# Performance work log

Hardware: AMD Instinct MI355X
Metric: run time of the kernel (lower is better)

The kernel has to match this reference:

```python
import jax, jax.numpy as jnp
import numpy as np

B, S, D, R = 256, 512, 128, 2048
H = 0.5  # integration step


def setup_inputs() -> dict:
    key = jax.random.key(0)
    ks = jax.random.split(key, 14)
    u = lambda k, shape, lo, hi: jax.random.uniform(k, shape, jnp.float32, lo, hi)
    bd, br = 1.0 / np.sqrt(D), 1.0 / np.sqrt(R)
    return {
        "inputs": jax.random.normal(ks[0], (B, S, D), jnp.float32),
        # input oscillator params (size D)
        "omega_in": u(ks[1], (D,), 1.0, 3.0),
        "gamma_in": u(ks[2], (D,), 0.1, 0.5),
        "alpha_in": u(ks[3], (D,), 0.5, 1.5),
        # input projection Linear(D -> R), torch layout [out, in]
        "W_proj": u(ks[4], (R, D), -bd, bd),
        "b_proj": u(ks[5], (R,), -bd, bd),
        # fixed reservoir oscillator params (size R)
        "omega_res": u(ks[6], (R,), 1.0, 3.0),
        "gamma_res": u(ks[7], (R,), 0.1, 0.5),
        "alpha_res": u(ks[8], (R,), 0.5, 1.5),
        # output oscillator params (size R)
        "omega_out": u(ks[9], (R,), 1.0, 3.0),
        "gamma_out": u(ks[10], (R,), 0.1, 0.5),
        "alpha_out": u(ks[11], (R,), 0.5, 1.5),
        # readout Linear(R -> D)
        "W_read": u(ks[12], (D, R), -br, br),
        "b_read": u(ks[13], (D,), -br, br),
    }


def _osc_step(f, x, y, omega, gamma, alpha):
    # x' = x + h*y ; y' = y + h*(alpha*f - 2|gamma|*y - |omega|^2 * x), clamped to [-5,5]
    accel = alpha * f - 2.0 * jnp.abs(gamma) * y - jnp.abs(omega) ** 2 * x
    x_new = jnp.clip(x + H * y, -5.0, 5.0)
    y_new = jnp.clip(y + H * accel, -5.0, 5.0)
    return x_new, y_new


def reference(inputs, omega_in, gamma_in, alpha_in, W_proj, b_proj,
              omega_res, gamma_res, alpha_res, omega_out, gamma_out, alpha_out,
              W_read, b_read):
    inputs_t = jnp.transpose(inputs, (1, 0, 2))  # [S, B, D]

    def step(carry, inp_t):
        x_in, y_in, x_res, y_res, x_out, y_out = carry
        x_in, y_in = _osc_step(inp_t, x_in, y_in, omega_in, gamma_in, alpha_in)
        proj = x_in @ W_proj.T + b_proj                      # [B, R]
        x_res, y_res = _osc_step(proj, x_res, y_res, omega_res, gamma_res, alpha_res)
        x_out, y_out = _osc_step(x_res, x_out, y_out, omega_out, gamma_out, alpha_out)
        pred = x_out @ W_read.T + b_read                     # [B, D]
        mse_out = jnp.mean((x_out - x_res) ** 2)             # scalar per step
        return (x_in, y_in, x_res, y_res, x_out, y_out), (pred, x_in, mse_out)

    z_d = jnp.zeros((B, D), inputs.dtype)
    z_r = jnp.zeros((B, R), inputs.dtype)
    carry0 = (z_d, z_d, z_r, z_r, z_r, z_r)
    _, (preds_t, x_in_seq, mse_out_seq) = jax.lax.scan(step, carry0, inputs_t)

    preds = jnp.transpose(preds_t, (1, 0, 2))  # [B, S, D]
    # pc_loss_in = sum_{t<S-1} mean((x_in(t) - inputs(t+1))^2)
    pc_loss_in = jnp.sum(jnp.mean((x_in_seq[:-1] - inputs_t[1:]) ** 2, axis=(1, 2)))
    pc_loss_out = jnp.sum(mse_out_seq)
    return preds, pc_loss_in, pc_loss_out
```

## Files before the change

### kernel.cpp

```cpp
#include <hip/hip_runtime.h>
#include <hip/hip_bf16.h>

#define Bn 256
#define Sn 512
#define Dn 128
#define Rn 2048
#define TB 32
#define NBLK (Sn / TB)
#define LDX 136
#define LDPs 1028
#define LDI 132
#define RG 1024

using bf16_t = __hip_bfloat16;
typedef short bf16x8 __attribute__((ext_vector_type(8)));
typedef float f32x4 __attribute__((ext_vector_type(4)));
typedef float f32x2 __attribute__((ext_vector_type(2)));

__device__ __forceinline__ f32x2 clip2(f32x2 v) {
  v = __builtin_elementwise_max(v, (f32x2)(-5.f));
  v = __builtin_elementwise_min(v, (f32x2)(5.f));
  return v;
}

__device__ __forceinline__ unsigned bf16rne(float f) {
  const unsigned u = __float_as_uint(f);
  return (u + 0x7fffu + ((u >> 16) & 1u)) >> 16;
}
__device__ __forceinline__ unsigned pack_bf16(f32x2 v) {
  return (bf16rne(v.y) << 16) | (bf16rne(v.x) & 0xffffu);
}

__global__ __launch_bounds__(256) void k_prep(const float* __restrict__ Wp,
                                              const float* __restrict__ Wr,
                                              bf16_t* __restrict__ Wp_b,
                                              bf16_t* __restrict__ Wr_b,
                                              float* __restrict__ losses) {
  const int i = blockIdx.x * 256 + threadIdx.x;
  Wp_b[i] = __float2bfloat16(Wp[i]);
  Wr_b[i] = __float2bfloat16(Wr[i]);
  if (i == 0) { losses[0] = 0.f; losses[1] = 0.f; }
}

__global__ __launch_bounds__(256) void k_zero(float* __restrict__ preds,
                                              const float* __restrict__ br) {
  const int i = blockIdx.x * 256 + threadIdx.x;
  const f32x4 bv = *(const f32x4*)(br + (i & 31) * 4);
  *((f32x4*)preds + i) = bv;
}

__global__ __launch_bounds__(512, 4) void k_fused(
    const float* __restrict__ inp,
    const float* __restrict__ om_i, const float* __restrict__ ga_i,
    const float* __restrict__ al_i,
    const bf16_t* __restrict__ Wp, const float* __restrict__ bp,
    const float* __restrict__ omr, const float* __restrict__ gar,
    const float* __restrict__ alr,
    const float* __restrict__ omo, const float* __restrict__ gao,
    const float* __restrict__ alo,
    const bf16_t* __restrict__ Wr,
    float* __restrict__ preds, float* __restrict__ losses) {
  __shared__ bf16_t Xs[TB * LDX];
  __shared__ bf16_t PX[TB * LDPs];
  __shared__ float bpS[RG];
  __shared__ float smi[8], smo[8];

  const int tid = threadIdx.x;
  const int b = blockIdx.x >> 1, g = blockIdx.x & 1;
  const int rbase = g * RG;
  const int wv = tid >> 6, lane = tid & 63;
  const int lr = lane & 15, lq = lane >> 4;

  for (int i = tid; i < RG; i += 512) bpS[i] = bp[rbase + i];

  float xi = 0.f, yi = 0.f, pc_in = 0.f;
  float w2i = 0.f, g2i = 0.f, ai = 0.f;
  if (tid < Dn) {
    w2i = om_i[tid] * om_i[tid];
    g2i = 2.f * fabsf(ga_i[tid]);
    ai = al_i[tid];
  }
  const float* inpb = inp + (size_t)b * Sn * Dn;

  const int rl = tid * 2;
  f32x2 xr = (f32x2)0.f, yr = (f32x2)0.f, xo = (f32x2)0.f, yo = (f32x2)0.f;
  f32x2 w2r, g2r, arv, w2o, g2o, aov;
  {
    f32x2 t;
    t = *(const f32x2*)(omr + rbase + rl); w2r = t * t;
    t = *(const f32x2*)(gar + rbase + rl); g2r = __builtin_elementwise_abs(t) * 2.f;
    arv = *(const f32x2*)(alr + rbase + rl);
    t = *(const f32x2*)(omo + rbase + rl); w2o = t * t;
    t = *(const f32x2*)(gao + rbase + rl); g2o = __builtin_elementwise_abs(t) * 2.f;
    aov = *(const f32x2*)(alo + rbase + rl);
  }
  f32x2 pc_out2 = (f32x2)0.f;

  float* Is = (float*)PX;

  __syncthreads();

  for (int blk = 0; blk < NBLK; ++blk) {
    const int t0 = blk * TB;

    {
      const float* src = inpb + (size_t)t0 * Dn;
      for (int i = tid; i < (TB * Dn) / 4; i += 512) {
        const int row = i >> 5, c4 = (i & 31) * 4;
        f32x4 v = __builtin_nontemporal_load((const f32x4*)(src + (size_t)row * Dn + c4));
        *(f32x4*)&Is[row * LDI + c4] = v;
      }
    }
    __syncthreads();

    if (tid < Dn) {
#pragma unroll
      for (int tt = 0; tt < TB; ++tt) {
        const float f = Is[tt * LDI + tid];
        if (t0 + tt > 0) { const float e = xi - f; pc_in += e * e; }
        const float accel = ai * f - g2i * yi - w2i * xi;
        const float xn = fminf(fmaxf(xi + 0.5f * yi, -5.f), 5.f);
        const float yn = fminf(fmaxf(yi + 0.5f * accel, -5.f), 5.f);
        Xs[tt * LDX + tid] = __float2bfloat16(xn);
        xi = xn; yi = yn;
      }
    }
    __syncthreads();

    {
      bf16x8 af[2][4];
#pragma unroll
      for (int i = 0; i < 2; ++i)
#pragma unroll
        for (int k = 0; k < 4; ++k)
          af[i][k] = *(const bf16x8*)&Xs[(i * 16 + lr) * LDX + k * 32 + lq * 8];

      const int lb = wv * 128;
      const bf16_t* wp_base = Wp + (size_t)(rbase + lb + lr) * Dn + lq * 8;
      bf16x8 bf[2][4];
#pragma unroll
      for (int k = 0; k < 4; ++k) {
        bf[0][k] = *(const bf16x8*)(wp_base + (size_t)0 * 16 * Dn + k * 32);
        bf[1][k] = *(const bf16x8*)(wp_base + (size_t)1 * 16 * Dn + k * 32);
      }
      for (int j = 0; j < 8; ++j) {
        const int pb = j & 1;
        f32x4 acc[2] = {(f32x4)0.f, (f32x4)0.f};
#pragma unroll
        for (int k = 0; k < 4; ++k) {
          acc[0] = __builtin_amdgcn_mfma_f32_16x16x32_bf16(af[0][k], bf[pb][k], acc[0], 0, 0, 0);
          acc[1] = __builtin_amdgcn_mfma_f32_16x16x32_bf16(af[1][k], bf[pb][k], acc[1], 0, 0, 0);
        }
        if (j + 2 < 8) {
#pragma unroll
          for (int k = 0; k < 4; ++k)
            bf[pb][k] = *(const bf16x8*)(wp_base + (size_t)(j + 2) * 16 * Dn + k * 32);
        }
        const int cl = lb + j * 16 + lr;
        const float bv = bpS[cl];
#pragma unroll
        for (int i = 0; i < 2; ++i)
#pragma unroll
          for (int r = 0; r < 4; ++r)
            PX[(i * 16 + lq * 4 + r) * LDPs + cl] = __float2bfloat16(acc[i][r] + bv);
      }
    }
    __syncthreads();

    {
      unsigned pk = *(unsigned*)&PX[0 * LDPs + rl];
      for (int tt = 0; tt < TB; ++tt) {
        unsigned pk_n = pk;
        if (tt + 1 < TB) pk_n = *(unsigned*)&PX[(tt + 1) * LDPs + rl];
        f32x2 pv;
        pv.x = __uint_as_float(pk << 16);
        pv.y = __uint_as_float(pk & 0xffff0000u);
        f32x2 acr = arv * pv - g2r * yr - w2r * xr;
        f32x2 xrn = clip2(xr + yr * 0.5f);
        f32x2 yrn = clip2(yr + acr * 0.5f);
        f32x2 aco = aov * xrn - g2o * yo - w2o * xo;
        f32x2 xon = clip2(xo + yo * 0.5f);
        f32x2 yon = clip2(yo + aco * 0.5f);
        f32x2 e = xon - xrn;
        pc_out2 += e * e;
        xr = xrn; yr = yrn; xo = xon; yo = yon;
        *(unsigned*)&PX[tt * LDPs + rl] = pack_bf16(xon);
        pk = pk_n;
      }
    }
    __syncthreads();

    {
      const int d0 = wv * 16;
      const bf16_t* wr_base = Wr + (size_t)(d0 + lr) * Rn + rbase + lq * 8;
      f32x4 acc[2][2] = {{(f32x4)0.f, (f32x4)0.f}, {(f32x4)0.f, (f32x4)0.f}};
      bf16x8 bcur = *(const bf16x8*)(wr_base);
#pragma unroll 2
      for (int k0 = 0; k0 < RG; k0 += 32) {
        bf16x8 bnxt = bcur;
        if (k0 + 32 < RG) bnxt = *(const bf16x8*)(wr_base + k0 + 32);
        const int par = (k0 >> 5) & 1;
        bf16x8 a0 = *(const bf16x8*)&PX[(0 + lr) * LDPs + k0 + lq * 8];
        bf16x8 a1 = *(const bf16x8*)&PX[(16 + lr) * LDPs + k0 + lq * 8];
        acc[0][par] = __builtin_amdgcn_mfma_f32_16x16x32_bf16(a0, bcur, acc[0][par], 0, 0, 0);
        acc[1][par] = __builtin_amdgcn_mfma_f32_16x16x32_bf16(a1, bcur, acc[1][par], 0, 0, 0);
        bcur = bnxt;
      }
      float* outb = preds + (size_t)b * Sn * Dn + (size_t)t0 * Dn;
      const int col = d0 + lr;
#pragma unroll
      for (int i = 0; i < 2; ++i) {
        f32x4 a = acc[i][0] + acc[i][1];
#pragma unroll
        for (int r = 0; r < 4; ++r) {
          const int row = i * 16 + lq * 4 + r;
          atomicAdd(outb + (size_t)row * Dn + col, a[r]);
        }
      }
    }
    __syncthreads();
  }

  float vi = pc_in;
  float vo = pc_out2.x + pc_out2.y;
#pragma unroll
  for (int o = 32; o > 0; o >>= 1) {
    vi += __shfl_down(vi, o, 64);
    vo += __shfl_down(vo, o, 64);
  }
  if (lane == 0) { smi[wv] = vi; smo[wv] = vo; }
  __syncthreads();
  if (tid == 0) {
    float si = 0.f, so = 0.f;
#pragma unroll
    for (int w = 0; w < 8; ++w) { si += smi[w]; so += smo[w]; }
    if (g == 0) atomicAdd(losses + 0, si * (1.f / ((float)Bn * (float)Dn)));
    atomicAdd(losses + 1, so * (1.f / ((float)Bn * (float)Rn)));
  }
}

extern "C" void kernel_launch(void* const* d_in, const int* in_sizes, int n_in,
                              void* d_out, int out_size, void* d_ws, size_t ws_size,
                              hipStream_t stream) {
  const float* inputs    = (const float*)d_in[0];
  const float* omega_in  = (const float*)d_in[1];
  const float* gamma_in  = (const float*)d_in[2];
  const float* alpha_in  = (const float*)d_in[3];
  const float* W_proj    = (const float*)d_in[4];
  const float* b_proj    = (const float*)d_in[5];
  const float* omega_res = (const float*)d_in[6];
  const float* gamma_res = (const float*)d_in[7];
  const float* alpha_res = (const float*)d_in[8];
  const float* omega_out = (const float*)d_in[9];
  const float* gamma_out = (const float*)d_in[10];
  const float* alpha_out = (const float*)d_in[11];
  const float* W_read    = (const float*)d_in[12];
  const float* b_read    = (const float*)d_in[13];

  float* out = (float*)d_out;
  float* losses = out + (size_t)Bn * Sn * Dn;

  bf16_t* Wp_b = (bf16_t*)d_ws;
  bf16_t* Wr_b = Wp_b + (size_t)Rn * Dn;

  k_prep<<<1024, 256, 0, stream>>>(W_proj, W_read, Wp_b, Wr_b, losses);
  k_zero<<<(Bn * Sn * Dn / 4) / 256, 256, 0, stream>>>(out, b_read);
  k_fused<<<Bn * 2, 512, 0, stream>>>(inputs, omega_in, gamma_in, alpha_in,
                                      Wp_b, b_proj,
                                      omega_res, gamma_res, alpha_res,
                                      omega_out, gamma_out, alpha_out,
                                      Wr_b, out, losses);
}
```

Baseline: 675.8 us.

## Use one 1024-thread block per batch row, dropping atomics and zero-init kernel

Each batch element is now processed by a single 1024-thread block covering the full reservoir width, instead of two 512-thread blocks that each handled half of it. Because one block now owns each readout output, the partial-sum atomicAdds and the separate bias-fill kernel are replaced by direct nontemporal stores with the bias added in place. The next input tile is also prefetched into registers during the readout phase. The trade-offs are half as many blocks, a larger shared-memory footprint (PX doubles in size), and 1024-thread blocks that may lower occupancy.

After: 952.3 us. 1.41x slower.

```diff
diff --git a/kernel.cpp b/kernel.cpp
--- a/kernel.cpp
+++ b/kernel.cpp
@@ -8,9 +8,10 @@
 #define TB 32
 #define NBLK (Sn / TB)
 #define LDX 136
-#define LDPs 1028
+#define LDP 2052
 #define LDI 132
-#define RG 1024
+#define NT 1024
+#define NW 16
 
 using bf16_t = __hip_bfloat16;
 typedef short bf16x8 __attribute__((ext_vector_type(8)));
@@ -42,14 +43,7 @@
   if (i == 0) { losses[0] = 0.f; losses[1] = 0.f; }
 }
 
-__global__ __launch_bounds__(256) void k_zero(float* __restrict__ preds,
-                                              const float* __restrict__ br) {
-  const int i = blockIdx.x * 256 + threadIdx.x;
-  const f32x4 bv = *(const f32x4*)(br + (i & 31) * 4);
-  *((f32x4*)preds + i) = bv;
-}
-
-__global__ __launch_bounds__(512, 4) void k_fused(
+__global__ __launch_bounds__(1024, 4) void k_fused(
     const float* __restrict__ inp,
     const float* __restrict__ om_i, const float* __restrict__ ga_i,
     const float* __restrict__ al_i,
@@ -58,20 +52,19 @@
     const float* __restrict__ alr,
     const float* __restrict__ omo, const float* __restrict__ gao,
     const float* __restrict__ alo,
-    const bf16_t* __restrict__ Wr,
+    const bf16_t* __restrict__ Wr, const float* __restrict__ br,
     float* __restrict__ preds, float* __restrict__ losses) {
   __shared__ bf16_t Xs[TB * LDX];
-  __shared__ bf16_t PX[TB * LDPs];
-  __shared__ float bpS[RG];
-  __shared__ float smi[8], smo[8];
+  __shared__ bf16_t PX[TB * LDP];
+  __shared__ float bpS[Rn];
+  __shared__ float smi[NW], smo[NW];
 
   const int tid = threadIdx.x;
-  const int b = blockIdx.x >> 1, g = blockIdx.x & 1;
-  const int rbase = g * RG;
+  const int b = blockIdx.x;
   const int wv = tid >> 6, lane = tid & 63;
   const int lr = lane & 15, lq = lane >> 4;
 
-  for (int i = tid; i < RG; i += 512) bpS[i] = bp[rbase + i];
+  for (int i = tid; i < Rn; i += NT) bpS[i] = bp[i];
 
   float xi = 0.f, yi = 0.f, pc_in = 0.f;
   float w2i = 0.f, g2i = 0.f, ai = 0.f;
@@ -87,30 +80,31 @@
   f32x2 w2r, g2r, arv, w2o, g2o, aov;
   {
     f32x2 t;
-    t = *(const f32x2*)(omr + rbase + rl); w2r = t * t;
-    t = *(const f32x2*)(gar + rbase + rl); g2r = __builtin_elementwise_abs(t) * 2.f;
-    arv = *(const f32x2*)(alr + rbase + rl);
-    t = *(const f32x2*)(omo + rbase + rl); w2o = t * t;
-    t = *(const f32x2*)(gao + rbase + rl); g2o = __builtin_elementwise_abs(t) * 2.f;
-    aov = *(const f32x2*)(alo + rbase + rl);
+    t = *(const f32x2*)(omr + rl); w2r = t * t;
+    t = *(const f32x2*)(gar + rl); g2r = __builtin_elementwise_abs(t) * 2.f;
+    arv = *(const f32x2*)(alr + rl);
+    t = *(const f32x2*)(omo + rl); w2o = t * t;
+    t = *(const f32x2*)(gao + rl); g2o = __builtin_elementwise_abs(t) * 2.f;
+    aov = *(const f32x2*)(alo + rl);
   }
   f32x2 pc_out2 = (f32x2)0.f;
 
+  const int dj = wv & 7, di = wv >> 3, d0 = dj * 16;
+  const float bco = br[d0 + lr];
+  const bf16_t* wr_base = Wr + (size_t)(d0 + lr) * Rn + lq * 8;
+
   float* Is = (float*)PX;
+  const int srow = tid >> 5, sc4 = (tid & 31) * 4;
+
+  f32x4 stg = __builtin_nontemporal_load(
+      (const f32x4*)(inpb + (size_t)srow * Dn + sc4));
 
   __syncthreads();
 
   for (int blk = 0; blk < NBLK; ++blk) {
     const int t0 = blk * TB;
 
-    {
-      const float* src = inpb + (size_t)t0 * Dn;
-      for (int i = tid; i < (TB * Dn) / 4; i += 512) {
-        const int row = i >> 5, c4 = (i & 31) * 4;
-        f32x4 v = __builtin_nontemporal_load((const f32x4*)(src + (size_t)row * Dn + c4));
-        *(f32x4*)&Is[row * LDI + c4] = v;
-      }
-    }
+    *(f32x4*)&Is[srow * LDI + sc4] = stg;
     __syncthreads();
 
     if (tid < Dn) {
@@ -136,7 +130,7 @@
           af[i][k] = *(const bf16x8*)&Xs[(i * 16 + lr) * LDX + k * 32 + lq * 8];
 
       const int lb = wv * 128;
-      const bf16_t* wp_base = Wp + (size_t)(rbase + lb + lr) * Dn + lq * 8;
+      const bf16_t* wp_base = Wp + (size_t)(lb + lr) * Dn + lq * 8;
       bf16x8 bf[2][4];
 #pragma unroll
       for (int k = 0; k < 4; ++k) {
@@ -162,16 +156,16 @@
         for (int i = 0; i < 2; ++i)
 #pragma unroll
           for (int r = 0; r < 4; ++r)
-            PX[(i * 16 + lq * 4 + r) * LDPs + cl] = __float2bfloat16(acc[i][r] + bv);
+            PX[(i * 16 + lq * 4 + r) * LDP + cl] = __float2bfloat16(acc[i][r] + bv);
       }
     }
     __syncthreads();
 
     {
-      unsigned pk = *(unsigned*)&PX[0 * LDPs + rl];
+      unsigned pk = *(unsigned*)&PX[0 * LDP + rl];
       for (int tt = 0; tt < TB; ++tt) {
         unsigned pk_n = pk;
-        if (tt + 1 < TB) pk_n = *(unsigned*)&PX[(tt + 1) * LDPs + rl];
+        if (tt + 1 < TB) pk_n = *(unsigned*)&PX[(tt + 1) * LDP + rl];
         f32x2 pv;
         pv.x = __uint_as_float(pk << 16);
         pv.y = __uint_as_float(pk & 0xffff0000u);
@@ -184,38 +178,34 @@
         f32x2 e = xon - xrn;
         pc_out2 += e * e;
         xr = xrn; yr = yrn; xo = xon; yo = yon;
-        *(unsigned*)&PX[tt * LDPs + rl] = pack_bf16(xon);
+        *(unsigned*)&PX[tt * LDP + rl] = pack_bf16(xon);
         pk = pk_n;
       }
     }
     __syncthreads();
 
     {
-      const int d0 = wv * 16;
-      const bf16_t* wr_base = Wr + (size_t)(d0 + lr) * Rn + rbase + lq * 8;
-      f32x4 acc[2][2] = {{(f32x4)0.f, (f32x4)0.f}, {(f32x4)0.f, (f32x4)0.f}};
+      if (blk + 1 < NBLK)
+        stg = __builtin_nontemporal_load(
+            (const f32x4*)(inpb + (size_t)(t0 + TB) * Dn + (size_t)srow * Dn + sc4));
+
+      f32x4 acc[2] = {(f32x4)0.f, (f32x4)0.f};
       bf16x8 bcur = *(const bf16x8*)(wr_base);
 #pragma unroll 2
-      for (int k0 = 0; k0 < RG; k0 += 32) {
+      for (int k0 = 0; k0 < Rn; k0 += 32) {
         bf16x8 bnxt = bcur;
-        if (k0 + 32 < RG) bnxt = *(const bf16x8*)(wr_base + k0 + 32);
+        if (k0 + 32 < Rn) bnxt = *(const bf16x8*)(wr_base + k0 + 32);
+        bf16x8 a = *(const bf16x8*)&PX[(di * 16 + lr) * LDP + k0 + lq * 8];
         const int par = (k0 >> 5) & 1;
-        bf16x8 a0 = *(const bf16x8*)&PX[(0 + lr) * LDPs + k0 + lq * 8];
-        bf16x8 a1 = *(const bf16x8*)&PX[(16 + lr) * LDPs + k0 + lq * 8];
-        acc[0][par] = __builtin_amdgcn_mfma_f32_16x16x32_bf16(a0, bcur, acc[0][par], 0, 0, 0);
-        acc[1][par] = __builtin_amdgcn_mfma_f32_16x16x32_bf16(a1, bcur, acc[1][par], 0, 0, 0);
+        acc[par] = __builtin_amdgcn_mfma_f32_16x16x32_bf16(a, bcur, acc[par], 0, 0, 0);
         bcur = bnxt;
       }
       float* outb = preds + (size_t)b * Sn * Dn + (size_t)t0 * Dn;
-      const int col = d0 + lr;
-#pragma unroll
-      for (int i = 0; i < 2; ++i) {
-        f32x4 a = acc[i][0] + acc[i][1];
-#pragma unroll
-        for (int r = 0; r < 4; ++r) {
-          const int row = i * 16 + lq * 4 + r;
-          atomicAdd(outb + (size_t)row * Dn + col, a[r]);
-        }
+      const f32x4 s = acc[0] + acc[1];
+#pragma unroll
+      for (int r = 0; r < 4; ++r) {
+        const int row = di * 16 + lq * 4 + r;
+        __builtin_nontemporal_store(s[r] + bco, outb + (size_t)row * Dn + d0 + lr);
       }
     }
     __syncthreads();
@@ -233,8 +223,8 @@
   if (tid == 0) {
     float si = 0.f, so = 0.f;
 #pragma unroll
-    for (int w = 0; w < 8; ++w) { si += smi[w]; so += smo[w]; }
-    if (g == 0) atomicAdd(losses + 0, si * (1.f / ((float)Bn * (float)Dn)));
+    for (int w = 0; w < NW; ++w) { si += smi[w]; so += smo[w]; }
+    atomicAdd(losses + 0, si * (1.f / ((float)Bn * (float)Dn)));
     atomicAdd(losses + 1, so * (1.f / ((float)Bn * (float)Rn)));
   }
 }
@@ -264,10 +254,9 @@
   bf16_t* Wr_b = Wp_b + (size_t)Rn * Dn;
 
   k_prep<<<1024, 256, 0, stream>>>(W_proj, W_read, Wp_b, Wr_b, losses);
-  k_zero<<<(Bn * Sn * Dn / 4) / 256, 256, 0, stream>>>(out, b_read);
-  k_fused<<<Bn * 2, 512, 0, stream>>>(inputs, omega_in, gamma_in, alpha_in,
-                                      Wp_b, b_proj,
-                                      omega_res, gamma_res, alpha_res,
-                                      omega_out, gamma_out, alpha_out,
-                                      Wr_b, out, losses);
-}
+  k_fused<<<Bn, NT, 0, stream>>>(inputs, omega_in, gamma_in, alpha_in,
+                                 Wp_b, b_proj,
+                                 omega_res, gamma_res, alpha_res,
+                                 omega_out, gamma_out, alpha_out,
+                                 Wr_b, b_read, out, losses);
+}
```

## Defer readout GEMM into next block to overlap with input oscillator, drop barriers

Applied to the files above, without the earlier changes.

The readout GEMM for the previous 32-step block now runs in the next iteration, while threads 0-127 integrate the input oscillator; a final call handles the last block. Since each wave's projection columns match the columns its own threads use in the reservoir recurrence, the barrier between those two phases is removed. The input staging through shared memory and its barrier are also removed, with threads reading the inputs straight from global memory. The projection bias is added in fp32 registers during the recurrence instead of being read from shared memory before bf16 rounding, and the block-index mapping now spreads the two R-halves across the grid. Together these cut barriers per block and keep the otherwise idle waves busy, at the cost of more register pressure and uncached global loads inside the serial input loop.

New measurement: 699.6 us. +3.5%, slower.

```diff
diff --git a/kernel.cpp b/kernel.cpp
--- a/kernel.cpp
+++ b/kernel.cpp
@@ -9,7 +9,6 @@
 #define NBLK (Sn / TB)
 #define LDX 136
 #define LDPs 1028
-#define LDI 132
 #define RG 1024
 
 using bf16_t = __hip_bfloat16;
@@ -62,16 +61,13 @@
     float* __restrict__ preds, float* __restrict__ losses) {
   __shared__ bf16_t Xs[TB * LDX];
   __shared__ bf16_t PX[TB * LDPs];
-  __shared__ float bpS[RG];
   __shared__ float smi[8], smo[8];
 
   const int tid = threadIdx.x;
-  const int b = blockIdx.x >> 1, g = blockIdx.x & 1;
+  const int b = blockIdx.x & 255, g = blockIdx.x >> 8;
   const int rbase = g * RG;
   const int wv = tid >> 6, lane = tid & 63;
   const int lr = lane & 15, lq = lane >> 4;
-
-  for (int i = tid; i < RG; i += 512) bpS[i] = bp[rbase + i];
 
   float xi = 0.f, yi = 0.f, pc_in = 0.f;
   float w2i = 0.f, g2i = 0.f, ai = 0.f;
@@ -84,7 +80,7 @@
 
   const int rl = tid * 2;
   f32x2 xr = (f32x2)0.f, yr = (f32x2)0.f, xo = (f32x2)0.f, yo = (f32x2)0.f;
-  f32x2 w2r, g2r, arv, w2o, g2o, aov;
+  f32x2 w2r, g2r, arv, w2o, g2o, aov, bpv;
   {
     f32x2 t;
     t = *(const f32x2*)(omr + rbase + rl); w2r = t * t;
@@ -93,30 +89,47 @@
     t = *(const f32x2*)(omo + rbase + rl); w2o = t * t;
     t = *(const f32x2*)(gao + rbase + rl); g2o = __builtin_elementwise_abs(t) * 2.f;
     aov = *(const f32x2*)(alo + rbase + rl);
+    bpv = *(const f32x2*)(bp + rbase + rl);
   }
   f32x2 pc_out2 = (f32x2)0.f;
 
-  float* Is = (float*)PX;
-
-  __syncthreads();
+  const bf16_t* wp_base = Wp + (size_t)(rbase + wv * 128 + lr) * Dn + lq * 8;
+  const int d0 = wv * 16;
+  const bf16_t* wr_base = Wr + (size_t)(d0 + lr) * Rn + rbase + lq * 8;
+
+  auto phaseD = [&](int tp0) {
+    f32x4 acc[2][2] = {{(f32x4)0.f, (f32x4)0.f}, {(f32x4)0.f, (f32x4)0.f}};
+    bf16x8 bcur = *(const bf16x8*)(wr_base);
+#pragma unroll 2
+    for (int k0 = 0; k0 < RG; k0 += 32) {
+      bf16x8 bnxt = bcur;
+      if (k0 + 32 < RG) bnxt = *(const bf16x8*)(wr_base + k0 + 32);
+      const int par = (k0 >> 5) & 1;
+      bf16x8 a0 = *(const bf16x8*)&PX[(0 + lr) * LDPs + k0 + lq * 8];
+      bf16x8 a1 = *(const bf16x8*)&PX[(16 + lr) * LDPs + k0 + lq * 8];
+      acc[0][par] = __builtin_amdgcn_mfma_f32_16x16x32_bf16(a0, bcur, acc[0][par], 0, 0, 0);
+      acc[1][par] = __builtin_amdgcn_mfma_f32_16x16x32_bf16(a1, bcur, acc[1][par], 0, 0, 0);
+      bcur = bnxt;
+    }
+    float* outb = preds + (size_t)b * Sn * Dn + (size_t)tp0 * Dn;
+#pragma unroll
+    for (int i = 0; i < 2; ++i) {
+      f32x4 s = acc[i][0] + acc[i][1];
+#pragma unroll
+      for (int r = 0; r < 4; ++r) {
+        const int row = i * 16 + lq * 4 + r;
+        atomicAdd(outb + (size_t)row * Dn + d0 + lr, s[r]);
+      }
+    }
+  };
 
   for (int blk = 0; blk < NBLK; ++blk) {
     const int t0 = blk * TB;
 
-    {
-      const float* src = inpb + (size_t)t0 * Dn;
-      for (int i = tid; i < (TB * Dn) / 4; i += 512) {
-        const int row = i >> 5, c4 = (i & 31) * 4;
-        f32x4 v = __builtin_nontemporal_load((const f32x4*)(src + (size_t)row * Dn + c4));
-        *(f32x4*)&Is[row * LDI + c4] = v;
-      }
-    }
-    __syncthreads();
-
     if (tid < Dn) {
 #pragma unroll
       for (int tt = 0; tt < TB; ++tt) {
-        const float f = Is[tt * LDI + tid];
+        const float f = inpb[(size_t)(t0 + tt) * Dn + tid];
         if (t0 + tt > 0) { const float e = xi - f; pc_in += e * e; }
         const float accel = ai * f - g2i * yi - w2i * xi;
         const float xn = fminf(fmaxf(xi + 0.5f * yi, -5.f), 5.f);
@@ -125,6 +138,7 @@
         xi = xn; yi = yn;
       }
     }
+    if (blk > 0) phaseD(t0 - TB);
     __syncthreads();
 
     {
@@ -135,37 +149,33 @@
         for (int k = 0; k < 4; ++k)
           af[i][k] = *(const bf16x8*)&Xs[(i * 16 + lr) * LDX + k * 32 + lq * 8];
 
-      const int lb = wv * 128;
-      const bf16_t* wp_base = Wp + (size_t)(rbase + lb + lr) * Dn + lq * 8;
-      bf16x8 bf[2][4];
+      bf16x8 bfr[2][4];
 #pragma unroll
       for (int k = 0; k < 4; ++k) {
-        bf[0][k] = *(const bf16x8*)(wp_base + (size_t)0 * 16 * Dn + k * 32);
-        bf[1][k] = *(const bf16x8*)(wp_base + (size_t)1 * 16 * Dn + k * 32);
+        bfr[0][k] = *(const bf16x8*)(wp_base + (size_t)0 * 16 * Dn + k * 32);
+        bfr[1][k] = *(const bf16x8*)(wp_base + (size_t)1 * 16 * Dn + k * 32);
       }
       for (int j = 0; j < 8; ++j) {
         const int pb = j & 1;
         f32x4 acc[2] = {(f32x4)0.f, (f32x4)0.f};
 #pragma unroll
         for (int k = 0; k < 4; ++k) {
-          acc[0] = __builtin_amdgcn_mfma_f32_16x16x32_bf16(af[0][k], bf[pb][k], acc[0], 0, 0, 0);
-          acc[1] = __builtin_amdgcn_mfma_f32_16x16x32_bf16(af[1][k], bf[pb][k], acc[1], 0, 0, 0);
+          acc[0] = __builtin_amdgcn_mfma_f32_16x16x32_bf16(af[0][k], bfr[pb][k], acc[0], 0, 0, 0);
+          acc[1] = __builtin_amdgcn_mfma_f32_16x16x32_bf16(af[1][k], bfr[pb][k], acc[1], 0, 0, 0);
         }
         if (j + 2 < 8) {
 #pragma unroll
           for (int k = 0; k < 4; ++k)
-            bf[pb][k] = *(const bf16x8*)(wp_base + (size_t)(j + 2) * 16 * Dn + k * 32);
+            bfr[pb][k] = *(const bf16x8*)(wp_base + (size_t)(j + 2) * 16 * Dn + k * 32);
         }
-        const int cl = lb + j * 16 + lr;
-        const float bv = bpS[cl];
+        const int cl = wv * 128 + j * 16 + lr;
 #pragma unroll
         for (int i = 0; i < 2; ++i)
 #pragma unroll
           for (int r = 0; r < 4; ++r)
-            PX[(i * 16 + lq * 4 + r) * LDPs + cl] = __float2bfloat16(acc[i][r] + bv);
-      }
-    }
-    __syncthreads();
+            PX[(i * 16 + lq * 4 + r) * LDPs + cl] = __float2bfloat16(acc[i][r]);
+      }
+    }
 
     {
       unsigned pk = *(unsigned*)&PX[0 * LDPs + rl];
@@ -175,6 +185,7 @@
         f32x2 pv;
         pv.x = __uint_as_float(pk << 16);
         pv.y = __uint_as_float(pk & 0xffff0000u);
+        pv += bpv;
         f32x2 acr = arv * pv - g2r * yr - w2r * xr;
         f32x2 xrn = clip2(xr + yr * 0.5f);
         f32x2 yrn = clip2(yr + acr * 0.5f);
@@ -189,37 +200,9 @@
       }
     }
     __syncthreads();
-
-    {
-      const int d0 = wv * 16;
-      const bf16_t* wr_base = Wr + (size_t)(d0 + lr) * Rn + rbase + lq * 8;
-      f32x4 acc[2][2] = {{(f32x4)0.f, (f32x4)0.f}, {(f32x4)0.f, (f32x4)0.f}};
-      bf16x8 bcur = *(const bf16x8*)(wr_base);
-#pragma unroll 2
-      for (int k0 = 0; k0 < RG; k0 += 32) {
-        bf16x8 bnxt = bcur;
-        if (k0 + 32 < RG) bnxt = *(const bf16x8*)(wr_base + k0 + 32);
-        const int par = (k0 >> 5) & 1;
-        bf16x8 a0 = *(const bf16x8*)&PX[(0 + lr) * LDPs + k0 + lq * 8];
-        bf16x8 a1 = *(const bf16x8*)&PX[(16 + lr) * LDPs + k0 + lq * 8];
-        acc[0][par] = __builtin_amdgcn_mfma_f32_16x16x32_bf16(a0, bcur, acc[0][par], 0, 0, 0);
-        acc[1][par] = __builtin_amdgcn_mfma_f32_16x16x32_bf16(a1, bcur, acc[1][par], 0, 0, 0);
-        bcur = bnxt;
-      }
-      float* outb = preds + (size_t)b * Sn * Dn + (size_t)t0 * Dn;
-      const int col = d0 + lr;
-#pragma unroll
-      for (int i = 0; i < 2; ++i) {
-        f32x4 a = acc[i][0] + acc[i][1];
-#pragma unroll
-        for (int r = 0; r < 4; ++r) {
-          const int row = i * 16 + lq * 4 + r;
-          atomicAdd(outb + (size_t)row * Dn + col, a[r]);
-        }
-      }
-    }
-    __syncthreads();
-  }
+  }
+
+  phaseD(Sn - TB);
 
   float vi = pc_in;
   float vo = pc_out2.x + pc_out2.y;
```
